# Kernel tuning notes

Hardware: AMD Instinct MI355X
Metric: run time of the kernel (lower is better)

The kernel has to match this reference:

```python
import jax, jax.numpy as jnp
import numpy as np

B, T, I, H, O = 16384, 512, 3, 32, 1

def setup_inputs() -> dict:
    key = jax.random.key(0)
    ks = jax.random.split(key, 7)
    s_ih = 1.0 / np.sqrt(H)
    return {
        "x": jax.random.normal(ks[0], (B, T, I), dtype=jnp.float32),
        # PyTorch LSTM params, gate order (i, f, g, o)
        "W_ih": jax.random.uniform(ks[1], (4 * H, I), jnp.float32, -s_ih, s_ih),
        "W_hh": jax.random.uniform(ks[2], (4 * H, H), jnp.float32, -s_ih, s_ih),
        "b_ih": jax.random.uniform(ks[3], (4 * H,), jnp.float32, -s_ih, s_ih),
        "b_hh": jax.random.uniform(ks[4], (4 * H,), jnp.float32, -s_ih, s_ih),
        "W_fc": jax.random.uniform(ks[5], (O, H), jnp.float32, -s_ih, s_ih),
        "b_fc": jax.random.uniform(ks[6], (O,), jnp.float32, -s_ih, s_ih),
    }

def _lstm_last_hidden(x, W_ih, W_hh, b_ih, b_hh):
    # Precompute input projections for all timesteps: [B, T, 4H]
    x_gates = jnp.einsum("bti,gi->btg", x, W_ih) + (b_ih + b_hh)

    def step(carry, xg_t):
        h, c = carry
        gates = xg_t + h @ W_hh.T  # [B, 4H]
        i_g, f_g, g_g, o_g = jnp.split(gates, 4, axis=-1)
        i_g = jax.nn.sigmoid(i_g)
        f_g = jax.nn.sigmoid(f_g)
        g_g = jnp.tanh(g_g)
        o_g = jax.nn.sigmoid(o_g)
        c = f_g * c + i_g * g_g
        h = o_g * jnp.tanh(c)
        return (h, c), None

    h0 = jnp.zeros((x.shape[0], W_hh.shape[1]), dtype=x.dtype)
    c0 = jnp.zeros_like(h0)
    # scan over time: xg time-major [T, B, 4H]
    (hT, _), _ = jax.lax.scan(step, (h0, c0), jnp.swapaxes(x_gates, 0, 1))
    return hT

def reference(x, W_ih, W_hh, b_ih, b_hh, W_fc, b_fc):
    hT = _lstm_last_hidden(x, W_ih, W_hh, b_ih, b_hh)  # [B, H]
    out = hT @ W_fc.T + b_fc  # [B, O]
    return jax.nn.sigmoid(out)
```

## Files before the change

### kernel.cpp

```cpp
#include <hip/hip_runtime.h>
#include <hip/hip_bf16.h>

typedef short bf16x8 __attribute__((ext_vector_type(8)));
typedef float f32x4 __attribute__((ext_vector_type(4)));
typedef unsigned int u32x4 __attribute__((ext_vector_type(4)));

#define MFMA(a, b, c) __builtin_amdgcn_mfma_f32_16x16x32_bf16((a), (b), (c), 0, 0, 0)

__device__ __forceinline__ unsigned short f2bf(float f) {
    unsigned u = __builtin_bit_cast(unsigned, f);
    unsigned r = u + 0x7FFFu + ((u >> 16) & 1u);
    return (unsigned short)(r >> 16);
}

__device__ __forceinline__ unsigned pk_bf16(float lo, float hi) {
    __hip_bfloat162 p = __float22bfloat162_rn(make_float2(lo, hi));
    unsigned r;
    __builtin_memcpy(&r, &p, sizeof(r));
    return r;
}

__device__ __forceinline__ float sigm(float x) {
    float e = __builtin_amdgcn_exp2f(-1.44269504088896f * x);
    return __builtin_amdgcn_rcpf(1.0f + e);
}

__global__ __launch_bounds__(256, 1) void lstm_mfma5_kernel(
    const float* __restrict__ x,
    const float* __restrict__ W_ih,
    const float* __restrict__ W_hh,
    const float* __restrict__ b_ih,
    const float* __restrict__ b_hh,
    const float* __restrict__ W_fc,
    const float* __restrict__ b_fc,
    float* __restrict__ out,
    int n_groups)
{
    const int lane  = threadIdx.x & 63;
    const int wid   = threadIdx.x >> 6;
    const int group = blockIdx.x * 4 + wid;
    if (group >= n_groups) return;

    const int n = lane & 15;
    const int q = lane >> 4;

    const float NL2E  = -1.4426950408889634f;
    const float P2L2E =  2.8853900817779268f;

    bf16x8 A_hh[8], A_x[8];
#pragma unroll
    for (int t = 0; t < 8; ++t) {
        const int g = 16 * t + n;
        const float s = (t == 4 || t == 5) ? P2L2E : NL2E;
        bf16x8 a, ax;
#pragma unroll
        for (int j = 0; j < 8; ++j) {
            const int k = 16 * (j >> 2) + 4 * q + (j & 3);
            a[j] = (short)f2bf(s * W_hh[g * 32 + k]);
            float axv = 0.0f;
            if (q == 0 && j < 4) {
                axv = (j < 3) ? s * W_ih[g * 3 + j] : s * (b_ih[g] + b_hh[g]);
            }
            ax[j] = (short)f2bf(axv);
        }
        A_hh[t] = a;
        A_x[t]  = ax;
    }

    const long bn = (long)group * 16 + n;
    const float4* xv = (const float4*)(x + bn * (512L * 3));

    float cs[8] = {0.f, 0.f, 0.f, 0.f, 0.f, 0.f, 0.f, 0.f};
    float h[8]  = {0.f, 0.f, 0.f, 0.f, 0.f, 0.f, 0.f, 0.f};
    bf16x8 Bh = {0, 0, 0, 0, 0, 0, 0, 0};

    float4 xa = xv[0], xb = xv[1], xc = xv[2];

    f32x4 accx[8];
    {
        unsigned bx01 = pk_bf16(xa.x, xa.y);
        unsigned bx23 = pk_bf16(xa.z, 1.0f);
        u32x4 bxv = {bx01, bx23, bx01, bx23};
        bf16x8 Bx = __builtin_bit_cast(bf16x8, bxv);
#pragma unroll
        for (int tt = 0; tt < 8; ++tt) {
            f32x4 z = {0.f, 0.f, 0.f, 0.f};
            accx[tt] = MFMA(A_x[tt], Bx, z);
        }
    }

#define STEP(XN0, XN1, XN2)                                                     \
    do {                                                                        \
        f32x4 acc[8];                                                           \
        _Pragma("unroll")                                                       \
        for (int tt = 0; tt < 8; ++tt) acc[tt] = MFMA(A_hh[tt], Bh, accx[tt]);  \
        unsigned bx01 = pk_bf16((XN0), (XN1));                                  \
        unsigned bx23 = pk_bf16((XN2), 1.0f);                                   \
        u32x4 bxv = {bx01, bx23, bx01, bx23};                                   \
        bf16x8 Bx = __builtin_bit_cast(bf16x8, bxv);                            \
        _Pragma("unroll")                                                       \
        for (int tt = 0; tt < 8; ++tt) {                                        \
            f32x4 z = {0.f, 0.f, 0.f, 0.f};                                     \
            accx[tt] = MFMA(A_x[tt], Bx, z);                                    \
        }                                                                       \
        _Pragma("unroll")                                                       \
        for (int r = 0; r < 4; ++r) {                                           \
            float ei0 = __builtin_amdgcn_exp2f(acc[0][r]);                      \
            float ef0 = __builtin_amdgcn_exp2f(acc[2][r]);                      \
            float eg0 = __builtin_amdgcn_exp2f(acc[4][r]);                      \
            float eo0 = __builtin_amdgcn_exp2f(acc[6][r]);                      \
            float ei1 = __builtin_amdgcn_exp2f(acc[1][r]);                      \
            float ef1 = __builtin_amdgcn_exp2f(acc[3][r]);                      \
            float eg1 = __builtin_amdgcn_exp2f(acc[5][r]);                      \
            float eo1 = __builtin_amdgcn_exp2f(acc[7][r]);                      \
            float a0 = 1.0f + ei0, b0 = 1.0f + ef0;                             \
            float c0 = 1.0f + eg0, d0 = 1.0f + eo0;                             \
            float a1 = 1.0f + ei1, b1 = 1.0f + ef1;                             \
            float c1 = 1.0f + eg1, d1 = 1.0f + eo1;                             \
            float rp0 = __builtin_amdgcn_rcpf(a0 * b0);                         \
            float rq0 = __builtin_amdgcn_rcpf(c0 * d0);                         \
            float rp1 = __builtin_amdgcn_rcpf(a1 * b1);                         \
            float rq1 = __builtin_amdgcn_rcpf(c1 * d1);                         \
            float ig0 = b0 * rp0, fg0 = a0 * rp0;                               \
            float rg0 = d0 * rq0, og0 = c0 * rq0;                               \
            float ig1 = b1 * rp1, fg1 = a1 * rp1;                               \
            float rg1 = d1 * rq1, og1 = c1 * rq1;                               \
            float gp0 = fmaf(-5.7707801635558536f, rg0, P2L2E);                 \
            float gp1 = fmaf(-5.7707801635558536f, rg1, P2L2E);                 \
            cs[r]     = fmaf(fg0, cs[r],     ig0 * gp0);                        \
            cs[4 + r] = fmaf(fg1, cs[4 + r], ig1 * gp1);                        \
            float ec0 = __builtin_amdgcn_exp2f(cs[r]);                          \
            float ec1 = __builtin_amdgcn_exp2f(cs[4 + r]);                      \
            float tc0 = fmaf(-2.0f, __builtin_amdgcn_rcpf(1.0f + ec0), 1.0f);   \
            float tc1 = fmaf(-2.0f, __builtin_amdgcn_rcpf(1.0f + ec1), 1.0f);   \
            h[r]      = og0 * tc0;                                              \
            h[4 + r]  = og1 * tc1;                                              \
        }                                                                       \
        u32x4 bhv = {pk_bf16(h[0], h[1]), pk_bf16(h[2], h[3]),                  \
                     pk_bf16(h[4], h[5]), pk_bf16(h[6], h[7])};                 \
        Bh = __builtin_bit_cast(bf16x8, bhv);                                   \
    } while (0)

    for (int w4 = 0; w4 < 128; ++w4) {
        const int nw = (w4 < 127) ? (w4 + 1) : 127;
        float4 na = xv[3 * nw + 0];
        float4 nb = xv[3 * nw + 1];
        float4 nc = xv[3 * nw + 2];

        STEP(xa.w, xb.x, xb.y);
        STEP(xb.z, xb.w, xc.x);
        STEP(xc.y, xc.z, xc.w);
        STEP(na.x, na.y, na.z);

        xa = na; xb = nb; xc = nc;
    }
#undef STEP

    float part = 0.f;
#pragma unroll
    for (int r = 0; r < 4; ++r) {
        part += W_fc[4 * q + r] * h[r];
        part += W_fc[16 + 4 * q + r] * h[4 + r];
    }
    part += __shfl_xor(part, 16, 64);
    part += __shfl_xor(part, 32, 64);
    if (q == 0) {
        out[bn] = sigm(part + b_fc[0]);
    }
}

extern "C" void kernel_launch(void* const* d_in, const int* in_sizes, int n_in,
                              void* d_out, int out_size, void* d_ws, size_t ws_size,
                              hipStream_t stream) {
    const float* x    = (const float*)d_in[0];
    const float* W_ih = (const float*)d_in[1];
    const float* W_hh = (const float*)d_in[2];
    const float* b_ih = (const float*)d_in[3];
    const float* b_hh = (const float*)d_in[4];
    const float* W_fc = (const float*)d_in[5];
    const float* b_fc = (const float*)d_in[6];
    float* out        = (float*)d_out;

    const int n_groups = out_size / 16;
    const int n_blocks = (n_groups + 3) / 4;

    hipLaunchKernelGGL(lstm_mfma5_kernel, dim3(n_blocks), dim3(256), 0, stream,
                       x, W_ih, W_hh, b_ih, b_hh, W_fc, b_fc, out, n_groups);
}
```

Measured before the change: 317.8 us.

## Halve batch per wavefront and split gate columns across lane halves via shuffles

Each wavefront now processes 8 batch rows instead of 16. The 16 MFMA columns are reorganised so that lanes 0-7 and 8-15 each take half of the hidden units for the same batch element, exchanging gate values and packed h through xor-8 shuffles. This halves the per-lane transcendental and elementwise work per step and doubles the number of wavefronts, with launch bounds raised to allow 2 blocks per CU for more latency hiding on the serial recurrence. The cost is twice the MFMA count per batch element plus extra cross-lane shuffles on the critical path.

```diff
diff --git a/kernel.cpp b/kernel.cpp
--- a/kernel.cpp
+++ b/kernel.cpp
@@ -25,7 +25,7 @@
     return __builtin_amdgcn_rcpf(1.0f + e);
 }
 
-__global__ __launch_bounds__(256, 1) void lstm_mfma5_kernel(
+__global__ __launch_bounds__(256, 2) void lstm_mfma7_kernel(
     const float* __restrict__ x,
     const float* __restrict__ W_ih,
     const float* __restrict__ W_hh,
@@ -41,8 +41,10 @@
     const int group = blockIdx.x * 4 + wid;
     if (group >= n_groups) return;
 
-    const int n = lane & 15;
-    const int q = lane >> 4;
+    const int n   = lane & 15;
+    const int q   = lane >> 4;
+    const int m   = n & 7;
+    const int hi8 = (n >> 3) & 1;
 
     const float NL2E  = -1.4426950408889634f;
     const float P2L2E =  2.8853900817779268f;
@@ -50,8 +52,10 @@
     bf16x8 A_hh[8], A_x[8];
 #pragma unroll
     for (int t = 0; t < 8; ++t) {
-        const int g = 16 * t + n;
-        const float s = (t == 4 || t == 5) ? P2L2E : NL2E;
+        const int G  = t >> 1;
+        const int ph = t & 1;
+        const int g  = 32 * G + 16 * ph + n;
+        const float s = (G == 2) ? P2L2E : NL2E;
         bf16x8 a, ax;
 #pragma unroll
         for (int j = 0; j < 8; ++j) {
@@ -67,12 +71,13 @@
         A_x[t]  = ax;
     }
 
-    const long bn = (long)group * 16 + n;
+    const long bn = (long)group * 8 + m;
     const float4* xv = (const float4*)(x + bn * (512L * 3));
 
-    float cs[8] = {0.f, 0.f, 0.f, 0.f, 0.f, 0.f, 0.f, 0.f};
-    float h[8]  = {0.f, 0.f, 0.f, 0.f, 0.f, 0.f, 0.f, 0.f};
+    float cs[4] = {0.f, 0.f, 0.f, 0.f};
+    float hr[4] = {0.f, 0.f, 0.f, 0.f};
     bf16x8 Bh = {0, 0, 0, 0, 0, 0, 0, 0};
+    const f32x4 z4 = {0.f, 0.f, 0.f, 0.f};
 
     float4 xa = xv[0], xb = xv[1], xc = xv[2];
 
@@ -83,61 +88,57 @@
         u32x4 bxv = {bx01, bx23, bx01, bx23};
         bf16x8 Bx = __builtin_bit_cast(bf16x8, bxv);
 #pragma unroll
-        for (int tt = 0; tt < 8; ++tt) {
-            f32x4 z = {0.f, 0.f, 0.f, 0.f};
-            accx[tt] = MFMA(A_x[tt], Bx, z);
-        }
+        for (int t = 0; t < 8; ++t) accx[t] = MFMA(A_x[t], Bx, z4);
     }
 
 #define STEP(XN0, XN1, XN2)                                                     \
     do {                                                                        \
+            \
         f32x4 acc[8];                                                           \
         _Pragma("unroll")                                                       \
-        for (int tt = 0; tt < 8; ++tt) acc[tt] = MFMA(A_hh[tt], Bh, accx[tt]);  \
+        for (int t = 0; t < 8; ++t) acc[t] = MFMA(A_hh[t], Bh, accx[t]);        \
+                    \
         unsigned bx01 = pk_bf16((XN0), (XN1));                                  \
         unsigned bx23 = pk_bf16((XN2), 1.0f);                                   \
         u32x4 bxv = {bx01, bx23, bx01, bx23};                                   \
         bf16x8 Bx = __builtin_bit_cast(bf16x8, bxv);                            \
         _Pragma("unroll")                                                       \
-        for (int tt = 0; tt < 8; ++tt) {                                        \
-            f32x4 z = {0.f, 0.f, 0.f, 0.f};                                     \
-            accx[tt] = MFMA(A_x[tt], Bx, z);                                    \
+        for (int t = 0; t < 8; ++t) accx[t] = MFMA(A_x[t], Bx, z4);             \
+                 \
+        float gv[4][4];                                                         \
+        _Pragma("unroll")                                                       \
+        for (int G = 0; G < 4; ++G) {                                           \
+            _Pragma("unroll")                                                   \
+            for (int r = 0; r < 4; ++r) {                                       \
+                float recv = __shfl_xor(acc[2 * G + 1][r], 8, 64);              \
+                gv[G][r] = hi8 ? recv : acc[2 * G][r];                          \
+            }                                                                   \
         }                                                                       \
+                                                 \
         _Pragma("unroll")                                                       \
         for (int r = 0; r < 4; ++r) {                                           \
-            float ei0 = __builtin_amdgcn_exp2f(acc[0][r]);                      \
-            float ef0 = __builtin_amdgcn_exp2f(acc[2][r]);                      \
-            float eg0 = __builtin_amdgcn_exp2f(acc[4][r]);                      \
-            float eo0 = __builtin_amdgcn_exp2f(acc[6][r]);                      \
-            float ei1 = __builtin_amdgcn_exp2f(acc[1][r]);                      \
-            float ef1 = __builtin_amdgcn_exp2f(acc[3][r]);                      \
-            float eg1 = __builtin_amdgcn_exp2f(acc[5][r]);                      \
-            float eo1 = __builtin_amdgcn_exp2f(acc[7][r]);                      \
-            float a0 = 1.0f + ei0, b0 = 1.0f + ef0;                             \
-            float c0 = 1.0f + eg0, d0 = 1.0f + eo0;                             \
-            float a1 = 1.0f + ei1, b1 = 1.0f + ef1;                             \
-            float c1 = 1.0f + eg1, d1 = 1.0f + eo1;                             \
-            float rp0 = __builtin_amdgcn_rcpf(a0 * b0);                         \
-            float rq0 = __builtin_amdgcn_rcpf(c0 * d0);                         \
-            float rp1 = __builtin_amdgcn_rcpf(a1 * b1);                         \
-            float rq1 = __builtin_amdgcn_rcpf(c1 * d1);                         \
-            float ig0 = b0 * rp0, fg0 = a0 * rp0;                               \
-            float rg0 = d0 * rq0, og0 = c0 * rq0;                               \
-            float ig1 = b1 * rp1, fg1 = a1 * rp1;                               \
-            float rg1 = d1 * rq1, og1 = c1 * rq1;                               \
-            float gp0 = fmaf(-5.7707801635558536f, rg0, P2L2E);                 \
-            float gp1 = fmaf(-5.7707801635558536f, rg1, P2L2E);                 \
-            cs[r]     = fmaf(fg0, cs[r],     ig0 * gp0);                        \
-            cs[4 + r] = fmaf(fg1, cs[4 + r], ig1 * gp1);                        \
-            float ec0 = __builtin_amdgcn_exp2f(cs[r]);                          \
-            float ec1 = __builtin_amdgcn_exp2f(cs[4 + r]);                      \
-            float tc0 = fmaf(-2.0f, __builtin_amdgcn_rcpf(1.0f + ec0), 1.0f);   \
-            float tc1 = fmaf(-2.0f, __builtin_amdgcn_rcpf(1.0f + ec1), 1.0f);   \
-            h[r]      = og0 * tc0;                                              \
-            h[4 + r]  = og1 * tc1;                                              \
+            float ei = __builtin_amdgcn_exp2f(gv[0][r]);                        \
+            float ef = __builtin_amdgcn_exp2f(gv[1][r]);                        \
+            float eg = __builtin_amdgcn_exp2f(gv[2][r]);                        \
+            float eo = __builtin_amdgcn_exp2f(gv[3][r]);                        \
+            float a1 = 1.0f + ei, b1 = 1.0f + ef;                               \
+            float c1 = 1.0f + eg, d1 = 1.0f + eo;                               \
+            float rp = __builtin_amdgcn_rcpf(a1 * b1);                          \
+            float rq = __builtin_amdgcn_rcpf(c1 * d1);                          \
+            float ig = b1 * rp, fg = a1 * rp;                                   \
+            float rg = d1 * rq, og = c1 * rq;                                   \
+            float gp = fmaf(-5.7707801635558536f, rg, P2L2E);                   \
+            cs[r] = fmaf(fg, cs[r], ig * gp);                                   \
+            float ec = __builtin_amdgcn_exp2f(cs[r]);                           \
+            float tc = fmaf(-2.0f, __builtin_amdgcn_rcpf(1.0f + ec), 1.0f);     \
+            hr[r] = og * tc;                                                    \
         }                                                                       \
-        u32x4 bhv = {pk_bf16(h[0], h[1]), pk_bf16(h[2], h[3]),                  \
-                     pk_bf16(h[4], h[5]), pk_bf16(h[6], h[7])};                 \
+                    \
+        unsigned p0 = pk_bf16(hr[0], hr[1]);                                    \
+        unsigned p1 = pk_bf16(hr[2], hr[3]);                                    \
+        unsigned r0 = __shfl_xor(p0, 8, 64);                                    \
+        unsigned r1 = __shfl_xor(p1, 8, 64);                                    \
+        u32x4 bhv = {p0, p1, r0, r1};                                           \
         Bh = __builtin_bit_cast(bf16x8, bhv);                                   \
     } while (0)
 
@@ -159,12 +160,12 @@
     float part = 0.f;
 #pragma unroll
     for (int r = 0; r < 4; ++r) {
-        part += W_fc[4 * q + r] * h[r];
-        part += W_fc[16 + 4 * q + r] * h[4 + r];
+        part += W_fc[16 * hi8 + 4 * q + r] * hr[r];
     }
+    part += __shfl_xor(part, 8, 64);
     part += __shfl_xor(part, 16, 64);
     part += __shfl_xor(part, 32, 64);
-    if (q == 0) {
+    if (lane == m) {
         out[bn] = sigm(part + b_fc[0]);
     }
 }
@@ -181,9 +182,9 @@
     const float* b_fc = (const float*)d_in[6];
     float* out        = (float*)d_out;
 
-    const int n_groups = out_size / 16;
+    const int n_groups = out_size / 8;
     const int n_blocks = (n_groups + 3) / 4;
 
-    hipLaunchKernelGGL(lstm_mfma5_kernel, dim3(n_blocks), dim3(256), 0, stream,
+    hipLaunchKernelGGL(lstm_mfma7_kernel, dim3(n_blocks), dim3(256), 0, stream,
                        x, W_ih, W_hh, b_ih, b_hh, W_fc, b_fc, out, n_groups);
 }
```

Measured after the change: 437.5 us. +37.7%, slower.
